# Kernel optimization log

Hardware: AMD Instinct MI355X
Metric: run time of the kernel (lower is better)

The kernel has to match this reference:

```python
import jax, jax.numpy as jnp
import numpy as np

B, L, D = 4, 2048, 1024
DI = D            # d_inner = expand * d_model, expand=1
N = 8             # d_state
K = 4             # d_conv
R = 64            # dt_rank = ceil(d_model/16)
EPS = 1e-5


def setup_inputs() -> dict:
    key = jax.random.key(0)
    ks = jax.random.split(key, 10)
    hidden_states = jax.random.normal(ks[0], (B, L, D), dtype=jnp.float32)
    norm_w = jnp.ones((D,), dtype=jnp.float32)
    in_proj_w = jax.random.normal(ks[1], (2 * DI, D), dtype=jnp.float32) * 0.02
    conv_w = jax.random.normal(ks[2], (DI, 1, K), dtype=jnp.float32) * 0.2
    conv_b = jnp.zeros((DI,), dtype=jnp.float32)
    x_proj_w = jax.random.normal(ks[3], (R + 2 * N, DI), dtype=jnp.float32) * 0.02
    dt_proj_w = jax.random.normal(ks[4], (DI, R), dtype=jnp.float32) * 0.1
    # bias init so softplus(bias) lands in a sane dt range (~e^-4 .. e^-1)
    dt_proj_b = jax.random.uniform(ks[5], (DI,), minval=-4.0, maxval=-1.0, dtype=jnp.float32)
    # S4D-real style init: A = -[1..N] per channel
    A_log = jnp.log(jnp.broadcast_to(jnp.arange(1, N + 1, dtype=jnp.float32), (DI, N)))
    D_skip = jnp.ones((DI,), dtype=jnp.float32)
    out_proj_w = jax.random.normal(ks[6], (D, DI), dtype=jnp.float32) * 0.02
    return {
        "hidden_states": hidden_states, "norm_w": norm_w,
        "in_proj_w": in_proj_w, "conv_w": conv_w, "conv_b": conv_b,
        "x_proj_w": x_proj_w, "dt_proj_w": dt_proj_w, "dt_proj_b": dt_proj_b,
        "A_log": A_log, "D_skip": D_skip, "out_proj_w": out_proj_w,
    }


def _rmsnorm(x, w):
    return x * jax.lax.rsqrt(jnp.mean(x * x, axis=-1, keepdims=True) + EPS) * w


def _mamba_block(hidden_states, norm_w, in_proj_w, conv_w, conv_b,
                 x_proj_w, dt_proj_w, dt_proj_b, A_log, D_skip, out_proj_w):
    x = _rmsnorm(hidden_states, norm_w)                      # [B,L,D]
    xz = jnp.einsum('bld,ed->ble', x, in_proj_w)             # [B,L,2*DI]
    x, z = jnp.split(xz, 2, axis=-1)                         # [B,L,DI] each
    # causal depthwise conv1d (torch pads d_conv-1 both sides then slices :L => left pad only)
    xc = jnp.transpose(x, (0, 2, 1))                         # [B,DI,L]
    k = conv_w.shape[-1]
    xc = jax.lax.conv_general_dilated(
        xc, conv_w, window_strides=(1,), padding=[(k - 1, 0)],
        dimension_numbers=('NCH', 'OIH', 'NCH'), feature_group_count=DI)
    x = jax.nn.silu(jnp.transpose(xc, (0, 2, 1)) + conv_b)   # [B,L,DI]
    # input-dependent dt, B, C
    dbl = jnp.einsum('bld,ed->ble', x, x_proj_w)             # [B,L,R+2N]
    dt, Bm, Cm = jnp.split(dbl, [R, R + N], axis=-1)
    dt = jax.nn.softplus(jnp.einsum('blr,dr->bld', dt, dt_proj_w) + dt_proj_b)  # [B,L,DI]
    A = -jnp.exp(A_log)                                      # [DI,N]
    dA = jnp.exp(dt[..., None] * A)                          # [B,L,DI,N]
    dBx = dt[..., None] * Bm[:, :, None, :] * x[..., None]   # [B,L,DI,N]

    def step(h, inp):
        a_t, bx_t, c_t = inp                                 # [B,DI,N],[B,DI,N],[B,N]
        h = a_t * h + bx_t
        y = jnp.einsum('bdn,bn->bd', h, c_t)
        return h, y

    h0 = jnp.zeros((hidden_states.shape[0], DI, N), dtype=x.dtype)
    _, ys = jax.lax.scan(step, h0, (jnp.transpose(dA, (1, 0, 2, 3)),
                                    jnp.transpose(dBx, (1, 0, 2, 3)),
                                    jnp.transpose(Cm, (1, 0, 2))))
    y = jnp.transpose(ys, (1, 0, 2)) + D_skip * x            # [B,L,DI]
    y = y * jax.nn.silu(z)
    out = jnp.einsum('bld,ed->ble', y, out_proj_w)           # [B,L,D]
    return out  # use_res=False


def reference(hidden_states, norm_w, in_proj_w, conv_w, conv_b,
              x_proj_w, dt_proj_w, dt_proj_b, A_log, D_skip, out_proj_w):
    return _mamba_block(hidden_states, norm_w, in_proj_w, conv_w, conv_b,
                        x_proj_w, dt_proj_w, dt_proj_b, A_log, D_skip, out_proj_w)
```

## Files before the change

kernel.cpp:

```cpp
#include <hip/hip_runtime.h>
#include <stdint.h>
#include <stddef.h>


typedef unsigned short u16;
typedef unsigned int u32;
typedef _Float16 f16;
typedef __attribute__((ext_vector_type(8))) _Float16 half8;
typedef __attribute__((ext_vector_type(4))) _Float16 half4;
typedef __attribute__((ext_vector_type(4))) float f32x4;

#define LSEQ 2048
#define DMODEL 1024
#define NSTATE 8
#define NCHUNK 64
#define CHUNKL 32
#define NROWS 8192
#define WS_NEED (115ull << 20)

__device__ __forceinline__ void gload_lds16(const void* g, void* l) {
    __builtin_amdgcn_global_load_lds((__attribute__((address_space(1))) void*)g,
                                     (__attribute__((address_space(3))) void*)l,
                                     16, 0, 0);
}

__global__ __launch_bounds__(256) void sentinel_kernel(float* __restrict__ out, int n) {
    int i = blockIdx.x * 256 + threadIdx.x;
    if (i < n) out[i] = 999.0f;
}

#define T0 524288
#define T1 20480
#define T2 16384
#define T3 262144
#define WCVT_BLK 3216
#define ZERO_BLK 640
__global__ __launch_bounds__(256) void prep_kernel(const float* __restrict__ s0,
                                                   const float* __restrict__ s1,
                                                   const float* __restrict__ s2,
                                                   const float* __restrict__ s3,
                                                   f16* __restrict__ d0, f16* __restrict__ d1,
                                                   f16* __restrict__ d2, f16* __restrict__ d3,
                                                   float* __restrict__ dblz,
                                                   const float* __restrict__ X,
                                                   const float* __restrict__ W,
                                                   f16* __restrict__ O) {
    const int bx = blockIdx.x;
    const int tid = threadIdx.x;
    if (bx < WCVT_BLK) {
        int idx = bx * 256 + tid;
        const float* s; f16* d; int i;
        if (idx < T0) { s = s0; d = d0; i = idx; }
        else if (idx < T0 + T1) { s = s1; d = d1; i = idx - T0; }
        else if (idx < T0 + T1 + T2) { s = s2; d = d2; i = idx - T0 - T1; }
        else { s = s3; d = d3; i = idx - T0 - T1 - T2; }
        f32x4 v = *(const f32x4*)(s + (size_t)i * 4);
        half4 o; o[0] = (f16)v[0]; o[1] = (f16)v[1]; o[2] = (f16)v[2]; o[3] = (f16)v[3];
        *(half4*)(d + (size_t)i * 4) = o;
    } else if (bx < WCVT_BLK + ZERO_BLK) {
        int i = (bx - WCVT_BLK) * 256 + tid;
        const f32x4 z4 = {0.f, 0.f, 0.f, 0.f};
        ((f32x4*)dblz)[i] = z4;
    } else {
        const int row = bx - (WCVT_BLK + ZERO_BLK);
        f32x4 u = *(const f32x4*)(X + (size_t)row * DMODEL + tid * 4);
        float ss = u[0]*u[0] + u[1]*u[1] + u[2]*u[2] + u[3]*u[3];
        for (int off = 32; off; off >>= 1) ss += __shfl_down(ss, off, 64);
        __shared__ float red[4];
        if ((tid & 63) == 0) red[tid >> 6] = ss;
        __syncthreads();
        float tot = red[0] + red[1] + red[2] + red[3];
        float scale = rsqrtf(tot * (1.0f / DMODEL) + 1e-5f);
        f32x4 w = *(const f32x4*)(W + tid * 4);
        half4 o;
        o[0] = (f16)(u[0] * scale * w[0]); o[1] = (f16)(u[1] * scale * w[1]);
        o[2] = (f16)(u[2] * scale * w[2]); o[3] = (f16)(u[3] * scale * w[3]);
        *(half4*)(O + (size_t)row * DMODEL + tid * 4) = o;
    }
}

template <int EPI, int AF32>
__global__ __launch_bounds__(256) void gemm_f16(const void* __restrict__ Ap, int lda,
                                                const f16* __restrict__ Bm, int ldb,
                                                void* __restrict__ C0, void* __restrict__ C1,
                                                int ldc, int N, int klen,
                                                const float* __restrict__ fbias) {
    __shared__ alignas(16) f16 sA[128 * 64];
    __shared__ alignas(16) f16 sB[128 * 64];
    const int tid = threadIdx.x;
    const int wave = tid >> 6, lane = tid & 63;
    const int wm = (wave >> 1) * 64, wn = (wave & 1) * 64;
    const int tm = blockIdx.x, tn = blockIdx.y;
    const int q = lane >> 4, cl = lane & 15;
    const int kbeg = blockIdx.z * klen;

    f32x4 acc[4][4];
    const f32x4 zero4 = {0.f, 0.f, 0.f, 0.f};
#pragma unroll
    for (int t = 0; t < 4; t++)
#pragma unroll
        for (int u = 0; u < 4; u++) acc[t][u] = zero4;

    int rS[4], gkS[4];
#pragma unroll
    for (int j = 0; j < 4; j++) {
        int c = wave * 256 + j * 64 + lane;
        rS[j] = c >> 3;
        gkS[j] = (c & 7) ^ (rS[j] & 7);
    }

    for (int k0 = kbeg; k0 < kbeg + klen; k0 += 64) {
        __syncthreads();
#pragma unroll
        for (int j = 0; j < 4; j++) {
            int ldsoff = (wave * 256 + j * 64) * 8;
            if (!AF32) {
                int ga = tm * 128 + rS[j];
                gload_lds16((const f16*)Ap + (size_t)ga * lda + k0 + gkS[j] * 8, sA + ldsoff);
            }
            int gb = tn * 128 + rS[j];
            if (gb >= N) gb = N - 1;
            gload_lds16(Bm + (size_t)gb * ldb + k0 + gkS[j] * 8, sB + ldsoff);
        }
        __syncthreads();

        half8 af[4][2], bf[4][2];
#pragma unroll
        for (int t = 0; t < 4; t++)
#pragma unroll
            for (int s = 0; s < 2; s++) {
                int m = wm + t * 16 + cl;
                int kc = s * 4 + q;
                if (AF32) {
                    const float* pa = (const float*)Ap + (size_t)(tm * 128 + m) * lda + k0 + kc * 8;
                    f32x4 v0 = *(const f32x4*)pa, v1 = *(const f32x4*)(pa + 4);
                    half8 a;
                    a[0] = (f16)v0[0]; a[1] = (f16)v0[1]; a[2] = (f16)v0[2]; a[3] = (f16)v0[3];
                    a[4] = (f16)v1[0]; a[5] = (f16)v1[1]; a[6] = (f16)v1[2]; a[7] = (f16)v1[3];
                    af[t][s] = a;
                } else {
                    af[t][s] = *(const half8*)(sA + m * 64 + ((kc ^ (m & 7)) << 3));
                }
                int n = wn + t * 16 + cl;
                bf[t][s] = *(const half8*)(sB + n * 64 + ((kc ^ (n & 7)) << 3));
            }
#pragma unroll
        for (int t = 0; t < 4; t++)
#pragma unroll
            for (int u = 0; u < 4; u++) {
                acc[t][u] = __builtin_amdgcn_mfma_f32_16x16x32_f16(af[t][0], bf[u][0], acc[t][u], 0, 0, 0);
                acc[t][u] = __builtin_amdgcn_mfma_f32_16x16x32_f16(af[t][1], bf[u][1], acc[t][u], 0, 0, 0);
            }
    }

    const int rowbase = tm * 128 + wm + q * 4;
    const int colbase = tn * 128 + wn + cl;
#pragma unroll
    for (int t = 0; t < 4; t++)
#pragma unroll
        for (int r = 0; r < 4; r++) {
            size_t rb_ = (size_t)(rowbase + t * 16 + r) * ldc;
            size_t rb1 = (size_t)(rowbase + t * 16 + r) * 1024;
#pragma unroll
            for (int u = 0; u < 4; u++) {
                int gcol = colbase + u * 16;
                float v = acc[t][u][r];
                if (EPI == 0) {
                    if (gcol < 1024) ((f16*)C0)[rb1 + gcol] = (f16)v;
                    else             ((f16*)C1)[rb1 + gcol - 1024] = (f16)v;
                } else if (EPI == 1) {
                    if (gcol < N) ((float*)C0)[rb_ + gcol] = v;
                } else if (EPI == 2) {
                    if (gcol < N) atomicAdd((float*)C0 + rb_ + gcol, v);
                } else {
                    if (gcol < N) {
                        float sv = v + fbias[gcol];
                        sv = (sv > 15.f) ? sv : log1pf(__expf(sv));
                        ((f16*)C0)[rb_ + gcol] = (f16)sv;
                    }
                }
            }
        }
}

template __global__ void gemm_f16<3, 1>(const void*, int, const f16*, int,
                                        void*, void*, int, int, int, const float*);

__global__ __launch_bounds__(256) void dtproj_kernel(const float* __restrict__ Ap,
                                                     const f16* __restrict__ Wt,
                                                     f16* __restrict__ Cd,
                                                     const float* __restrict__ fbias) {
    __shared__ alignas(16) f16 sW[128 * 64];
    const int tid = threadIdx.x;
    const int wave = tid >> 6, lane = tid & 63;
    const int q = lane >> 4, cl = lane & 15;
    const int tm = blockIdx.x, tn = blockIdx.y;

#pragma unroll
    for (int j = 0; j < 4; j++) {
        int c = wave * 256 + j * 64 + lane;
        int row = c >> 3;
        int kc = (c & 7) ^ (row & 7);
        gload_lds16(Wt + (size_t)(tn * 128 + row) * 64 + kc * 8,
                    sW + (wave * 256 + j * 64) * 8);
    }

    half8 af[2][2];
#pragma unroll
    for (int t = 0; t < 2; t++)
#pragma unroll
        for (int s = 0; s < 2; s++) {
            int m = wave * 32 + t * 16 + cl;
            const float* pa = Ap + (size_t)(tm * 128 + m) * 80 + (s * 4 + q) * 8;
            f32x4 v0 = *(const f32x4*)pa, v1 = *(const f32x4*)(pa + 4);
            half8 a;
            a[0] = (f16)v0[0]; a[1] = (f16)v0[1]; a[2] = (f16)v0[2]; a[3] = (f16)v0[3];
            a[4] = (f16)v1[0]; a[5] = (f16)v1[1]; a[6] = (f16)v1[2]; a[7] = (f16)v1[3];
            af[t][s] = a;
        }

    __syncthreads();

    f32x4 acc[2][8];
    const f32x4 zero4 = {0.f, 0.f, 0.f, 0.f};
#pragma unroll
    for (int t = 0; t < 2; t++)
#pragma unroll
        for (int fn = 0; fn < 8; fn++) acc[t][fn] = zero4;

#pragma unroll
    for (int fn = 0; fn < 8; fn++) {
        int n = fn * 16 + cl;
#pragma unroll
        for (int s = 0; s < 2; s++) {
            half8 bf = *(const half8*)(sW + n * 64 + (((s * 4 + q) ^ (n & 7)) << 3));
            acc[0][fn] = __builtin_amdgcn_mfma_f32_16x16x32_f16(af[0][s], bf, acc[0][fn], 0, 0, 0);
            acc[1][fn] = __builtin_amdgcn_mfma_f32_16x16x32_f16(af[1][s], bf, acc[1][fn], 0, 0, 0);
        }
    }

    const int rowb = tm * 128 + wave * 32 + q * 4;
    const int colb = tn * 128 + cl;
#pragma unroll
    for (int t = 0; t < 2; t++)
#pragma unroll
        for (int r = 0; r < 4; r++) {
            size_t ro = (size_t)(rowb + t * 16 + r) * 1024;
#pragma unroll
            for (int fn = 0; fn < 8; fn++) {
                int gc = colb + fn * 16;
                float sv = acc[t][fn][r] + fbias[gc];
                sv = (sv > 15.f) ? sv : log1pf(__expf(sv));
                Cd[ro + gc] = (f16)sv;
            }
        }
}

__global__ __launch_bounds__(256) void conv_silu_kernel(const f16* __restrict__ x,
                                                        const float* __restrict__ cw,
                                                        const float* __restrict__ cb,
                                                        f16* __restrict__ xc) {
    const int rg = blockIdx.x;
    const int d = blockIdx.y * 256 + threadIdx.x;
    const int row0 = rg * 4;
    const int l0 = row0 & (LSEQ - 1);
    float w0 = cw[d * 4], w1 = cw[d * 4 + 1], w2 = cw[d * 4 + 2], w3 = cw[d * 4 + 3];
    float bias = cb[d];
    float v[7];
#pragma unroll
    for (int j = 0; j < 7; j++) {
        int ll = l0 - 3 + j;
        v[j] = (ll >= 0) ? (float)x[(size_t)(row0 - 3 + j) * 1024 + d] : 0.f;
    }
#pragma unroll
    for (int i = 0; i < 4; i++) {
        float acc = bias + w0 * v[i] + w1 * v[i + 1] + w2 * v[i + 2] + w3 * v[i + 3];
        xc[(size_t)(row0 + i) * 1024 + d] = (f16)(acc / (1.f + __expf(-acc)));
    }
}

__global__ __launch_bounds__(256) void scan1_kernel(const f16* __restrict__ dt,
                                                    const f16* __restrict__ xc,
                                                    const float* __restrict__ dbl,
                                                    const float* __restrict__ A_log,
                                                    float* __restrict__ hF,
                                                    float* __restrict__ Pb) {
    const int d = blockIdx.x * 256 + threadIdx.x;
    const int c = blockIdx.y;
    const int b = blockIdx.z;
    __shared__ float sB[CHUNKL * NSTATE];
    sB[threadIdx.x] = dbl[(size_t)(b * LSEQ + c * CHUNKL + (threadIdx.x >> 3)) * 80 + 64 + (threadIdx.x & 7)];
    __syncthreads();
    f32x4 al0 = *(const f32x4*)(A_log + d * 8);
    f32x4 al1 = *(const f32x4*)(A_log + d * 8 + 4);
    float Aa[NSTATE];
#pragma unroll
    for (int n = 0; n < 4; n++) { Aa[n] = -__expf(al0[n]); Aa[n + 4] = -__expf(al1[n]); }
    float h[NSTATE], P[NSTATE];
#pragma unroll
    for (int n = 0; n < NSTATE; n++) { h[n] = 0.f; P[n] = 1.f; }
    const f16* pdt = dt + (size_t)(b * LSEQ + c * CHUNKL) * 1024 + d;
    const f16* pxc = xc + (size_t)(b * LSEQ + c * CHUNKL) * 1024 + d;
    for (int lb = 0; lb < CHUNKL; lb += 8) {
        float vdt[8], vxc[8];
#pragma unroll
        for (int j = 0; j < 8; j++) {
            vdt[j] = (float)pdt[(size_t)(lb + j) * 1024];
            vxc[j] = (float)pxc[(size_t)(lb + j) * 1024];
        }
#pragma unroll
        for (int j = 0; j < 8; j++) {
            float dtx = vdt[j] * vxc[j];
#pragma unroll
            for (int n = 0; n < NSTATE; n++) {
                float e = __expf(Aa[n] * vdt[j]);
                h[n] = e * h[n] + dtx * sB[(lb + j) * 8 + n];
                P[n] *= e;
            }
        }
    }
    size_t base = ((size_t)(c * 4 + b) * 1024 + d) * 8;
    f32x4 o;
    o[0]=h[0]; o[1]=h[1]; o[2]=h[2]; o[3]=h[3]; *(f32x4*)(hF + base) = o;
    o[0]=h[4]; o[1]=h[5]; o[2]=h[6]; o[3]=h[7]; *(f32x4*)(hF + base + 4) = o;
    o[0]=P[0]; o[1]=P[1]; o[2]=P[2]; o[3]=P[3]; *(f32x4*)(Pb + base) = o;
    o[0]=P[4]; o[1]=P[5]; o[2]=P[6]; o[3]=P[7]; *(f32x4*)(Pb + base + 4) = o;
}

__global__ __launch_bounds__(256) void combine_kernel(const float* __restrict__ hF,
                                                      const float* __restrict__ Pb,
                                                      float* __restrict__ h0) {
    int t = blockIdx.x * 256 + threadIdx.x;
    int n = t & 7, dd = (t >> 3) & 1023, b = t >> 13;
    size_t off = (size_t)(b * 1024 + dd) * 8 + n;
    float h = 0.f;
#pragma unroll 8
    for (int c = 0; c < NCHUNK; c++) {
        size_t idx = (size_t)c * 32768 + off;
        h0[idx] = h;
        h = fmaf(Pb[idx], h, hF[idx]);
    }
}

__global__ __launch_bounds__(256) void scan2_kernel(const f16* __restrict__ dt,
                                                    const f16* __restrict__ xc,
                                                    const float* __restrict__ dbl,
                                                    const float* __restrict__ A_log,
                                                    const float* __restrict__ h0,
                                                    const f16* __restrict__ z,
                                                    const float* __restrict__ Dsk,
                                                    f16* __restrict__ yout) {
    const int d = blockIdx.x * 256 + threadIdx.x;
    const int c = blockIdx.y;
    const int b = blockIdx.z;
    __shared__ float sB[CHUNKL * NSTATE];
    __shared__ float sC[CHUNKL * NSTATE];
    {
        size_t rb = (size_t)(b * LSEQ + c * CHUNKL + (threadIdx.x >> 3)) * 80;
        sB[threadIdx.x] = dbl[rb + 64 + (threadIdx.x & 7)];
        sC[threadIdx.x] = dbl[rb + 72 + (threadIdx.x & 7)];
    }
    __syncthreads();
    f32x4 al0 = *(const f32x4*)(A_log + d * 8);
    f32x4 al1 = *(const f32x4*)(A_log + d * 8 + 4);
    float Aa[NSTATE];
#pragma unroll
    for (int n = 0; n < 4; n++) { Aa[n] = -__expf(al0[n]); Aa[n + 4] = -__expf(al1[n]); }
    float h[NSTATE];
    {
        size_t base = ((size_t)(c * 4 + b) * 1024 + d) * 8;
        f32x4 h0a = *(const f32x4*)(h0 + base);
        f32x4 h0b = *(const f32x4*)(h0 + base + 4);
#pragma unroll
        for (int n = 0; n < 4; n++) { h[n] = h0a[n]; h[n + 4] = h0b[n]; }
    }
    const float dval = Dsk[d];
    const size_t rowoff = (size_t)(b * LSEQ + c * CHUNKL) * 1024 + d;
    const f16* pdt = dt + rowoff;
    const f16* pxc = xc + rowoff;
    const f16* pz  = z  + rowoff;
    f16* py = yout + rowoff;
    for (int lb = 0; lb < CHUNKL; lb += 8) {
        float vdt[8], vxc[8], vz[8];
#pragma unroll
        for (int j = 0; j < 8; j++) {
            vdt[j] = (float)pdt[(size_t)(lb + j) * 1024];
            vxc[j] = (float)pxc[(size_t)(lb + j) * 1024];
            vz[j]  = (float)pz[(size_t)(lb + j) * 1024];
        }
#pragma unroll
        for (int j = 0; j < 8; j++) {
            float dtx = vdt[j] * vxc[j];
            float y = 0.f;
#pragma unroll
            for (int n = 0; n < NSTATE; n++) {
                float e = __expf(Aa[n] * vdt[j]);
                h[n] = e * h[n] + dtx * sB[(lb + j) * 8 + n];
                y += h[n] * sC[(lb + j) * 8 + n];
            }
            y += dval * vxc[j];
            y *= vz[j] / (1.f + __expf(-vz[j]));
            py[(size_t)(lb + j) * 1024] = (f16)y;
        }
    }
}

extern "C" void kernel_launch(void* const* d_in, const int* in_sizes, int n_in,
                              void* d_out, int out_size, void* d_ws, size_t ws_size,
                              hipStream_t stream) {
    (void)in_sizes; (void)n_in;
    const float* hidden    = (const float*)d_in[0];
    const float* norm_w    = (const float*)d_in[1];
    const float* in_proj_w = (const float*)d_in[2];
    const float* conv_w    = (const float*)d_in[3];
    const float* conv_b    = (const float*)d_in[4];
    const float* x_proj_w  = (const float*)d_in[5];
    const float* dt_proj_w = (const float*)d_in[6];
    const float* dt_proj_b = (const float*)d_in[7];
    const float* A_log     = (const float*)d_in[8];
    const float* D_skip    = (const float*)d_in[9];
    const float* out_proj_w= (const float*)d_in[10];
    float* out = (float*)d_out;

    if (ws_size < WS_NEED) {
        sentinel_kernel<<<dim3((out_size + 255) / 256), 256, 0, stream>>>(out, out_size);
        return;
    }

    char* ws = (char*)d_ws;
    f16*   xn_h  = (f16*)(ws);
    f16*   xbuf_h= (f16*)(ws + (16ull << 20));
    f16*   zbuf_h= (f16*)(ws + (32ull << 20));
    f16*   xc_h  = (f16*)(ws + (48ull << 20));
    f16*   wih   = (f16*)(ws + (64ull << 20));
    f16*   woh   = (f16*)(ws + (68ull << 20));
    f16*   wxh   = (f16*)(ws + (70ull << 20));
    f16*   wdh   = (f16*)(ws + (70ull << 20) + (512ull << 10));
    float* dbl_f = (float*)(ws + (71ull << 20));
    f16*   dth   = (f16*)(ws + (75ull << 20));
    float* hF    = (float*)(ws + (91ull << 20));
    float* Pb    = (float*)(ws + (99ull << 20));
    float* h0    = (float*)(ws + (107ull << 20));
    f16*   y_h   = xn_h;

    prep_kernel<<<dim3(WCVT_BLK + ZERO_BLK + NROWS), 256, 0, stream>>>(
        in_proj_w, x_proj_w, dt_proj_w, out_proj_w, wih, wxh, wdh, woh,
        dbl_f, hidden, norm_w, xn_h);
    gemm_f16<0, 0><<<dim3(64, 16), 256, 0, stream>>>(xn_h, 1024, wih, 1024,
                                                     xbuf_h, zbuf_h, 1024, 2048, 1024, nullptr);
    conv_silu_kernel<<<dim3(NROWS / 4, 4), 256, 0, stream>>>(xbuf_h, conv_w, conv_b, xc_h);
    gemm_f16<2, 0><<<dim3(64, 1, 4), 256, 0, stream>>>(xc_h, 1024, wxh, 1024,
                                                       dbl_f, nullptr, 80, 80, 256, nullptr);
    dtproj_kernel<<<dim3(64, 8), 256, 0, stream>>>(dbl_f, wdh, dth, dt_proj_b);
    scan1_kernel<<<dim3(4, NCHUNK, 4), 256, 0, stream>>>(dth, xc_h, dbl_f, A_log, hF, Pb);
    combine_kernel<<<dim3(128), 256, 0, stream>>>(hF, Pb, h0);
    scan2_kernel<<<dim3(4, NCHUNK, 4), 256, 0, stream>>>(dth, xc_h, dbl_f, A_log, h0,
                                                         zbuf_h, D_skip, y_h);
    gemm_f16<1, 0><<<dim3(64, 8), 256, 0, stream>>>(y_h, 1024, woh, 1024,
                                                    out, nullptr, 1024, 1024, 1024, nullptr);
}
```

Baseline: 298.9 us.

## Replace in_proj GEMM with 256x256-tile 8-wave pipelined double-buffered kernel

```diff
diff --git a/kernel.cpp b/kernel.cpp
--- a/kernel.cpp
+++ b/kernel.cpp
@@ -79,6 +79,135 @@
     }
 }
 
+
+#define G4 asm volatile("s_waitcnt vmcnt(4)" ::: "memory")
+#define G2 asm volatile("s_waitcnt vmcnt(2)" ::: "memory")
+#define G0 asm volatile("s_waitcnt vmcnt(0)" ::: "memory")
+#define GN (void)0
+
+#define SA8(tt, hf) do { \
+    gload_lds16(aG + (size_t)(tt) * 64 + (size_t)(hf) * hA, \
+                sA + (((tt) & 1) * 16384) + (hf) * 8192 + ldsW); \
+    gload_lds16(aG + (size_t)(tt) * 64 + (size_t)(hf) * hA + rA, \
+                sA + (((tt) & 1) * 16384) + (hf) * 8192 + 4096 + ldsW); \
+} while (0)
+#define SB8(tt, hf) do { \
+    gload_lds16(bG + (size_t)(tt) * 64 + (size_t)(hf) * hB, \
+                sB + (((tt) & 1) * 16384) + (hf) * 8192 + ldsW); \
+    gload_lds16(bG + (size_t)(tt) * 64 + (size_t)(hf) * hB + rB, \
+                sB + (((tt) & 1) * 16384) + (hf) * 8192 + 4096 + ldsW); \
+} while (0)
+
+#define PHASE(MH, NH, STAGE_STMT, GUARD_STMT) do { \
+    half8 paf[4][2], pbf[2][2]; \
+    _Pragma("unroll") \
+    for (int f_ = 0; f_ < 4; f_++) { \
+        paf[f_][0] = *(const half8*)(sAb + rdA0 + ((MH) * 4 + f_) * 1024); \
+        paf[f_][1] = *(const half8*)(sAb + rdA1 + ((MH) * 4 + f_) * 1024); \
+    } \
+    _Pragma("unroll") \
+    for (int g_ = 0; g_ < 2; g_++) { \
+        pbf[g_][0] = *(const half8*)(sBb + rdB0 + ((NH) * 2 + g_) * 1024); \
+        pbf[g_][1] = *(const half8*)(sBb + rdB1 + ((NH) * 2 + g_) * 1024); \
+    } \
+    STAGE_STMT; \
+    GUARD_STMT; \
+    __builtin_amdgcn_s_barrier(); \
+    __builtin_amdgcn_sched_barrier(0); \
+    __builtin_amdgcn_s_setprio(1); \
+    _Pragma("unroll") \
+    for (int f_ = 0; f_ < 4; f_++) \
+        _Pragma("unroll") \
+        for (int g_ = 0; g_ < 2; g_++) { \
+            acc[(MH) * 4 + f_][(NH) * 2 + g_] = __builtin_amdgcn_mfma_f32_16x16x32_f16( \
+                paf[f_][0], pbf[g_][0], acc[(MH) * 4 + f_][(NH) * 2 + g_], 0, 0, 0); \
+            acc[(MH) * 4 + f_][(NH) * 2 + g_] = __builtin_amdgcn_mfma_f32_16x16x32_f16( \
+                paf[f_][1], pbf[g_][1], acc[(MH) * 4 + f_][(NH) * 2 + g_], 0, 0, 0); \
+        } \
+    __builtin_amdgcn_s_setprio(0); \
+    __builtin_amdgcn_s_barrier(); \
+    __builtin_amdgcn_sched_barrier(0); \
+} while (0)
+
+template <int EPI>
+__global__ __launch_bounds__(512, 2) void gemm8p(const f16* __restrict__ Ap, int lda,
+                                                 const f16* __restrict__ Bm, int ldb,
+                                                 void* __restrict__ C0, void* __restrict__ C1,
+                                                 int KT) {
+    __shared__ alignas(16) f16 sA[2 * 256 * 64];
+    __shared__ alignas(16) f16 sB[2 * 256 * 64];
+    const int tid = threadIdx.x;
+    const int wave = tid >> 6, lane = tid & 63;
+    const int wm = wave >> 2, wn = wave & 3;
+    const int cl = lane & 15, q = lane >> 4;
+    const int tm = blockIdx.x, tn = blockIdx.y;
+
+    const int srow = tid >> 3;
+    const int skc = (tid & 7) ^ (srow & 7);
+    const f16* aG = Ap + (size_t)(tm * 256 + srow) * lda + skc * 8;
+    const f16* bG = Bm + (size_t)(tn * 256 + srow) * ldb + skc * 8;
+    const size_t rA = (size_t)64 * lda, hA = (size_t)128 * lda;
+    const size_t rB = (size_t)64 * ldb, hB = (size_t)128 * ldb;
+    const int ldsW = wave * 512;
+
+    const int swz0 = (q ^ (cl & 7)) << 3;
+    const int swz1 = ((4 + q) ^ (cl & 7)) << 3;
+    const int rdA0 = (wm * 128 + cl) * 64 + swz0;
+    const int rdA1 = (wm * 128 + cl) * 64 + swz1;
+    const int rdB0 = (wn * 64 + cl) * 64 + swz0;
+    const int rdB1 = (wn * 64 + cl) * 64 + swz1;
+
+    f32x4 acc[8][4];
+    const f32x4 zero4 = {0.f, 0.f, 0.f, 0.f};
+#pragma unroll
+    for (int f = 0; f < 8; f++)
+#pragma unroll
+        for (int g = 0; g < 4; g++) acc[f][g] = zero4;
+
+    SA8(0, 0); SB8(0, 0); SA8(0, 1); SB8(0, 1);
+    G4;
+    __builtin_amdgcn_s_barrier();
+    __builtin_amdgcn_sched_barrier(0);
+
+    for (int t = 0; t < KT - 1; t++) {
+        const f16* sAb = sA + (t & 1) * 16384;
+        const f16* sBb = sB + (t & 1) * 16384;
+        PHASE(0, 0, SA8(t + 1, 0), G4);
+        PHASE(1, 0, SB8(t + 1, 0), G4);
+        PHASE(0, 1, SA8(t + 1, 1), GN);
+        PHASE(1, 1, SB8(t + 1, 1), G4);
+    }
+    {
+        const int t = KT - 1;
+        const f16* sAb = sA + (t & 1) * 16384;
+        const f16* sBb = sB + (t & 1) * 16384;
+        PHASE(0, 0, GN, G2);
+        PHASE(1, 0, GN, G0);
+        PHASE(0, 1, GN, GN);
+        PHASE(1, 1, GN, GN);
+    }
+
+    const int rowb = tm * 256 + wm * 128 + q * 4;
+    const int colb = tn * 256 + wn * 64 + cl;
+#pragma unroll
+    for (int f = 0; f < 8; f++)
+#pragma unroll
+        for (int r = 0; r < 4; r++) {
+            size_t ro = (size_t)(rowb + f * 16 + r) * 1024;
+#pragma unroll
+            for (int g = 0; g < 4; g++) {
+                int gc = colb + g * 16;
+                float v = acc[f][g][r];
+                if (EPI == 0) {
+                    if (gc < 1024) ((f16*)C0)[ro + gc] = (f16)v;
+                    else           ((f16*)C1)[ro + gc - 1024] = (f16)v;
+                } else {
+                    ((float*)C0)[ro + gc] = v;
+                }
+            }
+        }
+}
+
 template <int EPI, int AF32>
 __global__ __launch_bounds__(256) void gemm_f16(const void* __restrict__ Ap, int lda,
                                                 const f16* __restrict__ Bm, int ldb,
@@ -185,6 +314,8 @@
 
 template __global__ void gemm_f16<3, 1>(const void*, int, const f16*, int,
                                         void*, void*, int, int, int, const float*);
+template __global__ void gemm_f16<0, 0>(const void*, int, const f16*, int,
+                                        void*, void*, int, int, int, const float*);
 
 __global__ __launch_bounds__(256) void dtproj_kernel(const float* __restrict__ Ap,
                                                      const f16* __restrict__ Wt,
@@ -446,8 +577,8 @@
     prep_kernel<<<dim3(WCVT_BLK + ZERO_BLK + NROWS), 256, 0, stream>>>(
         in_proj_w, x_proj_w, dt_proj_w, out_proj_w, wih, wxh, wdh, woh,
         dbl_f, hidden, norm_w, xn_h);
-    gemm_f16<0, 0><<<dim3(64, 16), 256, 0, stream>>>(xn_h, 1024, wih, 1024,
-                                                     xbuf_h, zbuf_h, 1024, 2048, 1024, nullptr);
+    gemm8p<0><<<dim3(32, 8), 512, 0, stream>>>(xn_h, 1024, wih, 1024,
+                                               xbuf_h, zbuf_h, 16);
     conv_silu_kernel<<<dim3(NROWS / 4, 4), 256, 0, stream>>>(xbuf_h, conv_w, conv_b, xc_h);
     gemm_f16<2, 0><<<dim3(64, 1, 4), 256, 0, stream>>>(xc_h, 1024, wxh, 1024,
                                                        dbl_f, nullptr, 80, 80, 256, nullptr);
```

Result: faster. 292.7 us (-2.1%).
